# Performance work log

Measured on AMD Instinct MI355X. Metric: run time of the kernel, lower is better.

Reference implementation:

```python
import jax, jax.numpy as jnp
import numpy as np

EPS = 1e-8

def _layernorm(x, gamma, beta):
    mu = jnp.mean(x, axis=-1, keepdims=True)
    var = jnp.mean((x - mu) ** 2, axis=-1, keepdims=True)
    return (x - mu) * jax.lax.rsqrt(var + 1e-5) * gamma + beta

def setup_inputs() -> dict:
    key = jax.random.key(0)
    ks = jax.random.split(key, 8)
    B, T, E, H = 64, 512, 512, 2048  # T == E required by original matmul
    s = 1.0 / np.sqrt(E)
    return {
        "x": jax.random.normal(ks[0], (B, T, E), dtype=jnp.float32),
        "gamma1": jnp.ones((E,), jnp.float32),
        "beta1": jnp.zeros((E,), jnp.float32),
        "Wv": jax.random.normal(ks[1], (E, E), jnp.float32) * s,   # surrogate for quantum Vx circuit
        "Ww": jax.random.normal(ks[2], (E, E), jnp.float32) * s,   # surrogate for quantum xWx circuit
        "gamma2": jnp.ones((E,), jnp.float32),
        "beta2": jnp.zeros((E,), jnp.float32),
        "W1": jax.random.normal(ks[3], (E, H), jnp.float32) * s,
        "b1": jnp.zeros((H,), jnp.float32),
        "W2": jax.random.normal(ks[4], (H, E), jnp.float32) * (1.0 / np.sqrt(H)),
        "b2": jnp.zeros((E,), jnp.float32),
    }

def reference(x, gamma1, beta1, Wv, Ww, gamma2, beta2, W1, b1, W2, b2):
    # LN -> quantum-surrogate attention -> residual -> LN -> MLP -> residual
    inp = _layernorm(x, gamma1, beta1)                       # [B,T,E]
    # Quantum Vx surrogate: sampler returns probabilities (non-negative) -> squared projection
    vx = (jnp.einsum('bte,ef->btf', inp, Wv)) ** 2           # [B,T,E], >= 0
    # Quantum xWx surrogate: pairwise bilinear score, squared (probability-like)
    proj = jnp.einsum('bte,ef->btf', inp, Ww)                # [B,T,E]
    xwx = (jnp.einsum('bie,bje->bij', proj, inp)) ** 2       # [B,T,T], >= 0
    vx = jnp.sqrt(vx + EPS)
    xwx = jnp.sqrt(xwx + EPS)
    attn = jax.nn.softmax(xwx, axis=-1)                      # [B,T,T]
    # original: matmul(attn, vx.transpose(1,2)) -> out[b,i,k] = sum_j attn[b,i,j] * vx[b,k,j]
    t = jnp.einsum('bij,bkj->bik', attn, vx)                 # [B,T,T] (T == E)
    x = x + t
    h = _layernorm(x, gamma2, beta2)
    h = jax.nn.gelu(jnp.einsum('bte,eh->bth', h, W1) + b1)
    h = jnp.einsum('bth,he->bte', h, W2) + b2
    return x + h
```

## Files before the change

### kernel.cpp

```cpp
#include <hip/hip_runtime.h>

using f16x8 = __attribute__((ext_vector_type(8))) _Float16;
using f32x4 = __attribute__((ext_vector_type(4))) float;
using u16 = unsigned short;
using u32 = unsigned int;

__device__ __forceinline__ u16 f2h(float f) {
  union { _Float16 h; u16 u; } c;
  c.h = (_Float16)f;
  return c.u;
}
__device__ __forceinline__ uint4 pack8(const u16* h) {
  uint4 r;
  r.x = (u32)h[0] | ((u32)h[1] << 16);
  r.y = (u32)h[2] | ((u32)h[3] << 16);
  r.z = (u32)h[4] | ((u32)h[5] << 16);
  r.w = (u32)h[6] | ((u32)h[7] << 16);
  return r;
}
__device__ __forceinline__ float gelu_fast(float x) {
  float u2 = 1.5957691216057308f * (x + 0.044715f * x * x * x);
  return x / (1.0f + __expf(-u2));
}
__device__ __forceinline__ void gload16(const void* g, void* l) {
  __builtin_amdgcn_global_load_lds(
      (const __attribute__((address_space(1))) void*)g,
      (__attribute__((address_space(3))) void*)l, 16, 0, 0);
}

__global__ __launch_bounds__(256) void transpose_f16_kernel(
    const float* __restrict__ in, u16* __restrict__ out, int R, int C)
{
  __shared__ float t[32][33];
  const int lx = threadIdx.x & 31, ly = threadIdx.x >> 5;
  const int c0 = blockIdx.x << 5, r0 = blockIdx.y << 5;
  for (int i = ly; i < 32; i += 8)
    t[i][lx] = in[(long)(r0 + i) * C + c0 + lx];
  __syncthreads();
  for (int i = ly; i < 32; i += 8)
    out[(long)(c0 + i) * R + r0 + lx] = f2h(t[lx][i]);
}

__global__ __launch_bounds__(256) void ln_f16_kernel(
    const float* __restrict__ x, const float* __restrict__ gamma,
    const float* __restrict__ beta, u16* __restrict__ outH)
{
  const int row  = (blockIdx.x << 2) + (threadIdx.x >> 6);
  const int lane = threadIdx.x & 63;
  const float* xr = x + (long)row * 512 + lane * 8;
  float v[8];
  *(float4*)&v[0] = *(const float4*)xr;
  *(float4*)&v[4] = *(const float4*)(xr + 4);
  float s = 0.f;
#pragma unroll
  for (int j = 0; j < 8; ++j) s += v[j];
#pragma unroll
  for (int o = 32; o; o >>= 1) s += __shfl_xor(s, o);
  const float mu = s * (1.0f / 512.0f);
  float q = 0.f;
#pragma unroll
  for (int j = 0; j < 8; ++j) { float d = v[j] - mu; q += d * d; }
#pragma unroll
  for (int o = 32; o; o >>= 1) q += __shfl_xor(q, o);
  const float rs = rsqrtf(q * (1.0f / 512.0f) + 1e-5f);
  float gv[8], bv[8];
  *(float4*)&gv[0] = *(const float4*)(gamma + lane * 8);
  *(float4*)&gv[4] = *(const float4*)(gamma + lane * 8 + 4);
  *(float4*)&bv[0] = *(const float4*)(beta + lane * 8);
  *(float4*)&bv[4] = *(const float4*)(beta + lane * 8 + 4);
  u16 hs[8];
#pragma unroll
  for (int j = 0; j < 8; ++j)
    hs[j] = f2h((v[j] - mu) * rs * gv[j] + bv[j]);
  *(uint4*)(outH + (long)row * 512 + lane * 8) = pack8(hs);
}

__global__ __launch_bounds__(256) void softmax_kernel(
    const float* __restrict__ scores, u16* __restrict__ attn)
{
  const int row  = (blockIdx.x << 2) + (threadIdx.x >> 6);
  const int lane = threadIdx.x & 63;
  const float* sr = scores + (long)row * 512 + lane * 8;
  float v[8];
  *(float4*)&v[0] = *(const float4*)sr;
  *(float4*)&v[4] = *(const float4*)(sr + 4);
  float m = v[0];
#pragma unroll
  for (int j = 1; j < 8; ++j) m = fmaxf(m, v[j]);
#pragma unroll
  for (int o = 32; o; o >>= 1) m = fmaxf(m, __shfl_xor(m, o));
  float e[8], s = 0.f;
#pragma unroll
  for (int j = 0; j < 8; ++j) { e[j] = __expf(v[j] - m); s += e[j]; }
#pragma unroll
  for (int o = 32; o; o >>= 1) s += __shfl_xor(s, o);
  const float inv = 1.0f / s;
  u16 h[8];
#pragma unroll
  for (int j = 0; j < 8; ++j) h[j] = f2h(e[j] * inv);
  *(uint4*)(attn + (long)row * 512 + lane * 8) = pack8(h);
}

template<int EPI>
__global__ __launch_bounds__(1024) void gemm8(
    const char* A0, const char* A1, const char* A2, const char* A3,
    const char* B0, const char* B1, const char* B2, const char* B3,
    int N, int NT, int ldAb, int ldBb,
    long sAb, long sBb, long sC,
    float* __restrict__ outF, u16* __restrict__ outU,
    const float* __restrict__ resid, const float* __restrict__ bias)
{
  __shared__ __align__(16) char lds[131072];
  const int tid = threadIdx.x;
  const int w = tid >> 6, l = tid & 63;
  const int wm = w >> 2, wn = w & 3;

  const int gx = gridDim.x, gy = gridDim.y;
  int flat = ((int)blockIdx.z * gy + (int)blockIdx.y) * gx + (int)blockIdx.x;
  const int total = gx * gy * (int)gridDim.z;
  flat = (flat & 7) * (total >> 3) + (flat >> 3);
  const int bx = flat % gx;
  int rem = flat / gx;
  const int by = rem % gy, bz = rem / gy;

  const long blockM = (long)by * 256;
  const long blockN = (long)bx * 256;
  const long za = (long)bz * sAb;
  const long zb = (long)bz * sBb;
  const char* a0p = A0 + za; const char* a1p = A1 + za;
  const char* a2p = A2 + za; const char* a3p = A3 + za;
  const char* b0p = B0 + zb; const char* b1p = B1 + zb;
  const char* b2p = B2 + zb; const char* b3p = B3 + zb;

  auto partA = [&](int t) { return t < 8 ? a0p : t < 16 ? a1p : t < 24 ? a2p : a3p; };
  auto partB = [&](int t) { return t < 8 ? b0p : t < 16 ? b1p : t < 24 ? b2p : b3p; };

  const long stgSw = ((tid & 7) ^ ((tid >> 3) & 7)) << 4;
  const long raA = (blockM + (tid >> 3)) * (long)ldAb + stgSw;
  const long raB = (blockN + (tid >> 3)) * (long)ldBb + stgSw;
  auto stageA = [&](int t, int h) {
    const char* s = partA(t) + (((long)(t & 7)) << 7) + raA + (long)h * 128 * ldAb;
    gload16(s, lds + ((t & 1) << 15) + (h << 14) + (tid << 4));
  };
  auto stageB = [&](int t, int h) {
    const char* s = partB(t) + (((long)(t & 7)) << 7) + raB + (long)h * 128 * ldBb;
    gload16(s, lds + 65536 + ((t & 1) << 15) + (h << 14) + (tid << 4));
  };

  f32x4 acc[4][4];
#pragma unroll
  for (int i = 0; i < 4; ++i)
#pragma unroll
    for (int j = 0; j < 4; ++j) acc[i][j] = (f32x4){0.f, 0.f, 0.f, 0.f};

  const int lr = l & 15, kg = l >> 4;
  const int xs = kg ^ (l & 7);
  const int po0 = (lr << 7) + (xs << 4);
  const int po1 = (lr << 7) + ((xs ^ 4) << 4);
  const char* aL = lds + ((wm >> 1) << 14) + ((wm & 1) << 13);
  const char* bL = lds + 65536 + ((wn >> 1) << 14) + ((wn & 1) << 13);

  f16x8 a[4], b[4];
  auto readA = [&](const char* p) {
#pragma unroll
    for (int mf = 0; mf < 4; ++mf) a[mf] = *(const f16x8*)(p + (mf << 11));
  };
  auto readB = [&](const char* p) {
#pragma unroll
    for (int nf = 0; nf < 4; ++nf) b[nf] = *(const f16x8*)(p + (nf << 11));
  };

#define MFMA16()                                                              \
  do {                                                                        \
    _Pragma("unroll")                                                         \
    for (int mf = 0; mf < 4; ++mf)                                            \
      _Pragma("unroll")                                                       \
      for (int nf = 0; nf < 4; ++nf)                                          \
        acc[mf][nf] = __builtin_amdgcn_mfma_f32_16x16x32_f16(                 \
            b[nf], a[mf], acc[mf][nf], 0, 0, 0);                              \
  } while (0)

  stageA(0, 0); stageA(0, 1); stageB(0, 0); stageB(0, 1);
  __syncthreads();

  for (int t = 0; t < NT; ++t) {
    const int d = t & 1;
    const char* aD = aL + (d << 15);
    const char* bD = bL + (d << 15);
    if (t + 1 < NT) {
      stageA(t + 1, 0); stageA(t + 1, 1); stageB(t + 1, 0); stageB(t + 1, 1);
    }
    readA(aD + po0);
    readB(bD + po0);
    MFMA16();
    readA(aD + po1);
    readB(bD + po1);
    MFMA16();
    if (t + 1 < NT) __syncthreads();
  }
#undef MFMA16

  const long cb = (long)bz * sC;
  const int m0 = (int)blockM + wm * 64 + lr;
  const int n0 = (int)blockN + wn * 64 + (kg << 2);
#pragma unroll
  for (int mi = 0; mi < 4; ++mi)
#pragma unroll
    for (int ni = 0; ni < 4; ++ni) {
      const int m = m0 + (mi << 4);
      const int n = n0 + (ni << 4);
      const long idx = cb + (long)m * N + n;
      f32x4 v = acc[mi][ni];
      if (EPI == 0) {
        union { u16 h[4]; uint2 u; } p;
#pragma unroll
        for (int r = 0; r < 4; ++r) p.h[r] = f2h(sqrtf(v[r] * v[r] + 1e-8f));
        *(uint2*)(outU + idx) = p.u;
      } else if (EPI == 1) {
        union { u16 h[4]; uint2 u; } p;
#pragma unroll
        for (int r = 0; r < 4; ++r) p.h[r] = f2h(v[r]);
        *(uint2*)(outU + idx) = p.u;
      } else if (EPI == 2) {
        f32x4 o;
#pragma unroll
        for (int r = 0; r < 4; ++r) o[r] = sqrtf(v[r] * v[r] + 1e-8f);
        *(f32x4*)(outF + idx) = o;
      } else if (EPI == 3) {
        f32x4 rd = *(const f32x4*)(resid + idx);
#pragma unroll
        for (int r = 0; r < 4; ++r) rd[r] += v[r];
        *(f32x4*)(outF + idx) = rd;
      } else if (EPI == 4) {
        f32x4 bb = *(const f32x4*)(bias + n);
        union { u16 h[4]; uint2 u; } p;
#pragma unroll
        for (int r = 0; r < 4; ++r) p.h[r] = f2h(gelu_fast(v[r] + bb[r]));
        *(uint2*)(outU + idx) = p.u;
      } else {
        f32x4 rd = *(const f32x4*)(resid + idx);
        f32x4 bb = *(const f32x4*)(bias + n);
#pragma unroll
        for (int r = 0; r < 4; ++r) rd[r] += v[r] + bb[r];
        *(f32x4*)(outF + idx) = rd;
      }
    }
}

extern "C" void kernel_launch(void* const* d_in, const int* in_sizes, int n_in,
                              void* d_out, int out_size, void* d_ws, size_t ws_size,
                              hipStream_t stream)
{
  const float* x   = (const float*)d_in[0];
  const float* g1  = (const float*)d_in[1];
  const float* be1 = (const float*)d_in[2];
  const float* Wv  = (const float*)d_in[3];
  const float* Ww  = (const float*)d_in[4];
  const float* g2  = (const float*)d_in[5];
  const float* be2 = (const float*)d_in[6];
  const float* W1  = (const float*)d_in[7];
  const float* b1  = (const float*)d_in[8];
  const float* W2  = (const float*)d_in[9];
  const float* b2  = (const float*)d_in[10];
  float* out = (float*)d_out;

  char* ws = (char*)d_ws;
  u16* inp    = (u16*)(ws);
  u16* proj   = (u16*)(ws + 33554432);
  float* scores = (float*)(ws + 67108864);
  u16* vx     = (u16*)(ws + 134217728);
  u16* attn   = proj;
  u16* h_in   = inp;
  u16* h_mid  = (u16*)(ws + 33554432);
  char* wb = ws + 167772160;
  u16* WvT = (u16*)(wb);
  u16* WwT = (u16*)(wb + 524288);
  u16* W1T = (u16*)(wb + 1048576);
  u16* W2T = (u16*)(wb + 3145728);

  transpose_f16_kernel<<<dim3(16, 16), 256, 0, stream>>>(Wv, WvT, 512, 512);
  transpose_f16_kernel<<<dim3(16, 16), 256, 0, stream>>>(Ww, WwT, 512, 512);
  transpose_f16_kernel<<<dim3(64, 16), 256, 0, stream>>>(W1, W1T, 512, 2048);
  transpose_f16_kernel<<<dim3(16, 64), 256, 0, stream>>>(W2, W2T, 2048, 512);

  ln_f16_kernel<<<8192, 256, 0, stream>>>(x, g1, be1, inp);

  gemm8<1><<<dim3(2, 128, 1), 1024, 0, stream>>>(
      (const char*)inp, (const char*)inp, (const char*)inp, (const char*)inp,
      (const char*)WwT, (const char*)WwT, (const char*)WwT, (const char*)WwT,
      512, 8, 1024, 1024, 0, 0, 0,
      nullptr, proj, nullptr, nullptr);

  gemm8<2><<<dim3(2, 2, 64), 1024, 0, stream>>>(
      (const char*)proj, (const char*)proj, (const char*)proj, (const char*)proj,
      (const char*)inp, (const char*)inp, (const char*)inp, (const char*)inp,
      512, 8, 1024, 1024, 524288, 524288, 262144,
      scores, nullptr, nullptr, nullptr);

  softmax_kernel<<<8192, 256, 0, stream>>>(scores, attn);

  gemm8<0><<<dim3(2, 128, 1), 1024, 0, stream>>>(
      (const char*)inp, (const char*)inp, (const char*)inp, (const char*)inp,
      (const char*)WvT, (const char*)WvT, (const char*)WvT, (const char*)WvT,
      512, 8, 1024, 1024, 0, 0, 0,
      nullptr, vx, nullptr, nullptr);

  gemm8<3><<<dim3(2, 2, 64), 1024, 0, stream>>>(
      (const char*)attn, (const char*)attn, (const char*)attn, (const char*)attn,
      (const char*)vx, (const char*)vx, (const char*)vx, (const char*)vx,
      512, 8, 1024, 1024, 524288, 524288, 262144,
      out, nullptr, x, nullptr);

  ln_f16_kernel<<<8192, 256, 0, stream>>>(out, g2, be2, h_in);

  gemm8<4><<<dim3(8, 128, 1), 1024, 0, stream>>>(
      (const char*)h_in, (const char*)h_in, (const char*)h_in, (const char*)h_in,
      (const char*)W1T, (const char*)W1T, (const char*)W1T, (const char*)W1T,
      2048, 8, 1024, 1024, 0, 0, 0,
      nullptr, h_mid, nullptr, b1);

  gemm8<5><<<dim3(2, 128, 1), 1024, 0, stream>>>(
      (const char*)h_mid, (const char*)h_mid + 1024, (const char*)h_mid + 2048, (const char*)h_mid + 3072,
      (const char*)W2T, (const char*)W2T + 1024, (const char*)W2T + 2048, (const char*)W2T + 3072,
      512, 32, 4096, 4096, 0, 0, 0,
      out, nullptr, out, b2);
}
```

Baseline: 368.8 us.

## Fuse Ww and Wv projections into one GEMM and store scores in fp16

Concatenates the transposed Ww and Wv weights so a single N=1024 GEMM produces both proj and sqrt-abs vx into one interleaved buffer, with a new epilogue that applies the sqrt only to the Wv half. The score GEMM now writes fp16 with the sqrt epilogue instead of fp32, and the softmax reads fp16, which halves score traffic. Downstream GEMMs use strided views into the combined buffer. This saves a launch, one pass over the input and score bandwidth, at the risk of fp16 rounding in the pre-softmax scores.

```diff
diff --git a/kernel.cpp b/kernel.cpp
--- a/kernel.cpp
+++ b/kernel.cpp
@@ -75,15 +75,15 @@
   *(uint4*)(outH + (long)row * 512 + lane * 8) = pack8(hs);
 }
 
-__global__ __launch_bounds__(256) void softmax_kernel(
-    const float* __restrict__ scores, u16* __restrict__ attn)
+__global__ __launch_bounds__(256) void softmax_f16_kernel(
+    const u16* __restrict__ scores, u16* __restrict__ attn)
 {
   const int row  = (blockIdx.x << 2) + (threadIdx.x >> 6);
   const int lane = threadIdx.x & 63;
-  const float* sr = scores + (long)row * 512 + lane * 8;
+  const f16x8 v8 = *(const f16x8*)(scores + (long)row * 512 + lane * 8);
   float v[8];
-  *(float4*)&v[0] = *(const float4*)sr;
-  *(float4*)&v[4] = *(const float4*)(sr + 4);
+#pragma unroll
+  for (int j = 0; j < 8; ++j) v[j] = (float)v8[j];
   float m = v[0];
 #pragma unroll
   for (int j = 1; j < 8; ++j) m = fmaxf(m, v[j]);
@@ -203,6 +203,7 @@
   const long cb = (long)bz * sC;
   const int m0 = (int)blockM + wm * 64 + lr;
   const int n0 = (int)blockN + wn * 64 + (kg << 2);
+  const bool vabs = (blockN >= 512);
 #pragma unroll
   for (int mi = 0; mi < 4; ++mi)
 #pragma unroll
@@ -237,12 +238,18 @@
 #pragma unroll
         for (int r = 0; r < 4; ++r) p.h[r] = f2h(gelu_fast(v[r] + bb[r]));
         *(uint2*)(outU + idx) = p.u;
-      } else {
+      } else if (EPI == 5) {
         f32x4 rd = *(const f32x4*)(resid + idx);
         f32x4 bb = *(const f32x4*)(bias + n);
 #pragma unroll
         for (int r = 0; r < 4; ++r) rd[r] += v[r] + bb[r];
         *(f32x4*)(outF + idx) = rd;
+      } else {
+        union { u16 h[4]; uint2 u; } p;
+#pragma unroll
+        for (int r = 0; r < 4; ++r)
+          p.h[r] = f2h(vabs ? sqrtf(v[r] * v[r] + 1e-8f) : v[r]);
+        *(uint2*)(outU + idx) = p.u;
       }
     }
 }
@@ -265,50 +272,43 @@
   float* out = (float*)d_out;
 
   char* ws = (char*)d_ws;
-  u16* inp    = (u16*)(ws);
-  u16* proj   = (u16*)(ws + 33554432);
-  float* scores = (float*)(ws + 67108864);
-  u16* vx     = (u16*)(ws + 134217728);
-  u16* attn   = proj;
-  u16* h_in   = inp;
-  u16* h_mid  = (u16*)(ws + 33554432);
+  u16* inp     = (u16*)(ws);
+  u16* pvx     = (u16*)(ws + 33554432);
+  u16* scores16= (u16*)(ws + 100663296);
+  u16* attn    = (u16*)(ws + 134217728);
+  u16* h_in    = inp;
+  u16* h_mid   = (u16*)(ws + 33554432);
   char* wb = ws + 167772160;
-  u16* WvT = (u16*)(wb);
-  u16* WwT = (u16*)(wb + 524288);
+  u16* WwT = (u16*)(wb);
+  u16* WvT = (u16*)(wb + 524288);
   u16* W1T = (u16*)(wb + 1048576);
   u16* W2T = (u16*)(wb + 3145728);
 
+  transpose_f16_kernel<<<dim3(16, 16), 256, 0, stream>>>(Ww, WwT, 512, 512);
   transpose_f16_kernel<<<dim3(16, 16), 256, 0, stream>>>(Wv, WvT, 512, 512);
-  transpose_f16_kernel<<<dim3(16, 16), 256, 0, stream>>>(Ww, WwT, 512, 512);
   transpose_f16_kernel<<<dim3(64, 16), 256, 0, stream>>>(W1, W1T, 512, 2048);
   transpose_f16_kernel<<<dim3(16, 64), 256, 0, stream>>>(W2, W2T, 2048, 512);
 
   ln_f16_kernel<<<8192, 256, 0, stream>>>(x, g1, be1, inp);
 
-  gemm8<1><<<dim3(2, 128, 1), 1024, 0, stream>>>(
+  gemm8<6><<<dim3(4, 128, 1), 1024, 0, stream>>>(
       (const char*)inp, (const char*)inp, (const char*)inp, (const char*)inp,
       (const char*)WwT, (const char*)WwT, (const char*)WwT, (const char*)WwT,
-      512, 8, 1024, 1024, 0, 0, 0,
-      nullptr, proj, nullptr, nullptr);
-
-  gemm8<2><<<dim3(2, 2, 64), 1024, 0, stream>>>(
-      (const char*)proj, (const char*)proj, (const char*)proj, (const char*)proj,
+      1024, 8, 1024, 1024, 0, 0, 0,
+      nullptr, pvx, nullptr, nullptr);
+
+  gemm8<0><<<dim3(2, 2, 64), 1024, 0, stream>>>(
+      (const char*)pvx, (const char*)pvx, (const char*)pvx, (const char*)pvx,
       (const char*)inp, (const char*)inp, (const char*)inp, (const char*)inp,
-      512, 8, 1024, 1024, 524288, 524288, 262144,
-      scores, nullptr, nullptr, nullptr);
-
-  softmax_kernel<<<8192, 256, 0, stream>>>(scores, attn);
-
-  gemm8<0><<<dim3(2, 128, 1), 1024, 0, stream>>>(
-      (const char*)inp, (const char*)inp, (const char*)inp, (const char*)inp,
-      (const char*)WvT, (const char*)WvT, (const char*)WvT, (const char*)WvT,
-      512, 8, 1024, 1024, 0, 0, 0,
-      nullptr, vx, nullptr, nullptr);
+      512, 8, 2048, 1024, 1048576, 524288, 262144,
+      nullptr, scores16, nullptr, nullptr);
+
+  softmax_f16_kernel<<<8192, 256, 0, stream>>>(scores16, attn);
 
   gemm8<3><<<dim3(2, 2, 64), 1024, 0, stream>>>(
       (const char*)attn, (const char*)attn, (const char*)attn, (const char*)attn,
-      (const char*)vx, (const char*)vx, (const char*)vx, (const char*)vx,
-      512, 8, 1024, 1024, 524288, 524288, 262144,
+      (const char*)pvx + 1024, (const char*)pvx + 1024, (const char*)pvx + 1024, (const char*)pvx + 1024,
+      512, 8, 1024, 2048, 524288, 1048576, 262144,
       out, nullptr, x, nullptr);
 
   ln_f16_kernel<<<8192, 256, 0, stream>>>(out, g2, be2, h_in);
```

After: 362.1 us. Within noise of the previous version (-1.8%).
